# Performance work log

Hardware: AMD Instinct MI355X
Metric: run time of the kernel (lower is better)

Reference implementation:

```python
import jax, jax.numpy as jnp
import numpy as np

H = 64; H2 = 32; B = 256; NPART = 64
NP = B * NPART          # 16384 part nodes
PER_TF = 512            # torque/force nodes per graph
NT = B * PER_TF; NF = NT
E = 262144              # edges per edge type
L = 5; T = 4            # 4 main hetero layers + 1 actor layer; 4 edge types
NEG = 0.2; EPS = 1e-5


def _seg_softmax(e, seg, n):
    # softmax over entries sharing the same segment id (along axis 0)
    m = jax.lax.stop_gradient(jax.ops.segment_max(e, seg, num_segments=n))
    ex = jnp.exp(e - m[seg])
    s = jax.ops.segment_sum(ex, seg, num_segments=n)
    return ex / s[seg]


def _gat(x_s, x_d, es, ed, Ws, Wd, a_s, a_d, b, n_dst):
    # PyG GATConv, heads=1, add_self_loops=False, bipartite (x_src, x_dst)
    hs = x_s @ Ws                      # [Ns,H]
    hd = x_d @ Wd                      # [Nd,H]
    e = jax.nn.leaky_relu((hs @ a_s)[es] + (hd @ a_d)[ed], NEG)   # [E]
    al = _seg_softmax(e, ed, n_dst)                                # attn per dst neighborhood
    return jax.ops.segment_sum(al[:, None] * hs[es], ed, num_segments=n_dst) + b


def _hetero_layer(xp, xt, xf, edges, Ws, Wd, a_s, a_d, b):
    # to_hetero(aggr='sum'): one GATConv per edge type, sum into each dst type
    (pts, ptd), (tps, tpd), (pfs, pfd), (fps, fpd) = edges
    out_t = _gat(xp, xt, pts, ptd, Ws[0], Wd[0], a_s[0], a_d[0], b[0], xt.shape[0])
    out_p = (_gat(xt, xp, tps, tpd, Ws[1], Wd[1], a_s[1], a_d[1], b[1], xp.shape[0])
             + _gat(xf, xp, fps, fpd, Ws[3], Wd[3], a_s[3], a_d[3], b[3], xp.shape[0]))
    out_f = _gat(xp, xf, pfs, pfd, Ws[2], Wd[2], a_s[2], a_d[2], b[2], xf.shape[0])
    return out_p, out_t, out_f


def _pool(x):
    # MultiAggregation([max, min, mean]); segments are uniform -> reshape
    xr = x.reshape(B, -1, x.shape[-1])
    return jnp.concatenate([xr.max(1), xr.min(1), xr.mean(1)], axis=-1)


def reference(mass, part_state, torque_x, force_x,
              e_pt_src, e_pt_dst, e_tp_src, e_tp_dst,
              e_pf_src, e_pf_dst, e_fp_src, e_fp_dst,
              batch, part_id,
              emb_parts_W, emb_state, W_src, W_dst, a_src, a_dst, b_conv,
              ln_gamma, ln_beta, out_a_W, out_a_b,
              innet_W, innet_b, full_W, full_b, outnet_W, outnet_b):
    edges = ((e_pt_src, e_pt_dst), (e_tp_src, e_tp_dst),
             (e_pf_src, e_pf_dst), (e_fp_src, e_fp_dst))
    idx = part_state[:, 0] + 2 * part_state[:, 1]
    xp = jnp.concatenate([mass @ emb_parts_W, emb_state[idx]], axis=-1)  # [NP,H]
    xt, xf = torque_x, force_x
    for l in range(4):  # main hetero GAT, ReLU between layers, none after last
        xp, xt, xf = _hetero_layer(xp, xt, xf, edges,
                                   W_src[l], W_dst[l], a_src[l], a_dst[l], b_conv[l])
        if l < 3:
            xp, xt, xf = jax.nn.relu(xp), jax.nn.relu(xt), jax.nn.relu(xf)
    # actor: 1-layer hetero GAT (no activation)
    ap, at, af = _hetero_layer(xp, xt, xf, edges,
                               W_src[4], W_dst[4], a_src[4], a_dst[4], b_conv[4])
    # node LayerNorm
    mu = ap.mean(-1, keepdims=True)
    var = ((ap - mu) ** 2).mean(-1, keepdims=True)
    ra = (ap - mu) / jnp.sqrt(var + EPS) * ln_gamma + ln_beta
    ra = ra @ out_a_W + out_a_b                         # [NP,2]
    soft = _seg_softmax(ra, batch, B)                   # softmax per graph, per channel
    actions = jnp.zeros((B, 2, NPART), dtype=ra.dtype).at[batch, :, part_id].set(soft)
    actions = actions.reshape(B, 2 * NPART)
    rep = jnp.concatenate([_pool(xp), _pool(xt), _pool(xf)], axis=1)   # [B, 9H]
    repV = jax.nn.gelu(rep @ innet_W + innet_b, approximate=False)
    repV = jax.nn.gelu(repV @ full_W + full_b, approximate=False)
    V = jnp.tanh(repV @ outnet_W + outnet_b)            # [B,1]
    return actions, V


def setup_inputs():
    key = jax.random.key(0)
    ks = iter(jax.random.split(key, 40))
    f32 = jnp.float32
    inp = {}
    inp['mass'] = jax.random.uniform(next(ks), (NP, 1), dtype=f32)
    inp['part_state'] = jax.random.randint(next(ks), (NP, 2), 0, 2, dtype=jnp.int32)
    inp['torque_x'] = jax.random.normal(next(ks), (NT, H), dtype=f32)
    inp['force_x'] = jax.random.normal(next(ks), (NF, H), dtype=f32)
    for name, n in [('e_pt_src', NP), ('e_pt_dst', NT), ('e_tp_src', NT), ('e_tp_dst', NP),
                    ('e_pf_src', NP), ('e_pf_dst', NF), ('e_fp_src', NF), ('e_fp_dst', NP)]:
        inp[name] = jax.random.randint(next(ks), (E,), 0, n, dtype=jnp.int32)
    inp['batch'] = (jnp.arange(NP) // NPART).astype(jnp.int32)
    inp['part_id'] = (jnp.arange(NP) % NPART).astype(jnp.int32)
    s = 1.0 / np.sqrt(H)
    inp['emb_parts_W'] = jax.random.normal(next(ks), (1, H2), dtype=f32)
    inp['emb_state'] = jax.random.normal(next(ks), (4, H2), dtype=f32)
    inp['W_src'] = jax.random.normal(next(ks), (L, T, H, H), dtype=f32) * s
    inp['W_dst'] = jax.random.normal(next(ks), (L, T, H, H), dtype=f32) * s
    inp['a_src'] = jax.random.normal(next(ks), (L, T, H), dtype=f32) * s
    inp['a_dst'] = jax.random.normal(next(ks), (L, T, H), dtype=f32) * s
    inp['b_conv'] = jax.random.normal(next(ks), (L, T, H), dtype=f32) * 0.01
    inp['ln_gamma'] = jnp.ones((H,), dtype=f32)
    inp['ln_beta'] = jnp.zeros((H,), dtype=f32)
    inp['out_a_W'] = jax.random.normal(next(ks), (H, 2), dtype=f32) * s
    inp['out_a_b'] = jnp.zeros((2,), dtype=f32)
    inp['innet_W'] = jax.random.normal(next(ks), (9 * H, H), dtype=f32) / np.sqrt(9.0 * H)
    inp['innet_b'] = jnp.zeros((H,), dtype=f32)
    inp['full_W'] = jax.random.normal(next(ks), (H, H), dtype=f32) * s
    inp['full_b'] = jnp.zeros((H,), dtype=f32)
    inp['outnet_W'] = jax.random.normal(next(ks), (H, 1), dtype=f32) * s
    inp['outnet_b'] = jnp.zeros((1,), dtype=f32)
    return inp
```

## Files before the change

kernel.cpp:

```cpp
#include <hip/hip_runtime.h>
#include <math.h>

#define NP_ 16384
#define NT_ 131072
#define NF_ 131072
#define E_  262144
#define B_  256
#define NDTOT 294912
#define E4_  1048576

#define D0 0
#define D1 131072
#define D2 147456
#define D3 278528
#define S0 0
#define S1 16384
#define S2 147456
#define S3 163840

__device__ __forceinline__ float dot4(float4 a, float4 b) {
  return a.x * b.x + a.y * b.y + a.z * b.z + a.w * b.w;
}

__device__ __forceinline__ void gather2(
    int kb0, int ke0, float ad0, const float* __restrict__ aS0, const float* __restrict__ x0,
    int kb1, int ke1, float ad1, const float* __restrict__ aS1, const float* __restrict__ x1,
    const int* __restrict__ sortsrc, int q, int lanebase,
    float4* __restrict__ acc0o, float* __restrict__ si0o,
    float4* __restrict__ acc1o, float* __restrict__ si1o) {
  float4 acc0 = make_float4(0.f, 0.f, 0.f, 0.f);
  float4 acc1 = make_float4(0.f, 0.f, 0.f, 0.f);
  float m0 = -3e38f, m1 = -3e38f, sum0 = 0.f, sum1 = 0.f;
  int len = max(ke0 - kb0, ke1 - kb1);
  for (int c = 0; c < len; c += 16) {
    int k0 = kb0 + c + q, k1 = kb1 + c + q;
    int v0 = k0 < ke0, v1 = k1 < ke1;
    int sx0 = v0 ? sortsrc[k0] : 0;
    int sx1 = v1 ? sortsrc[k1] : 0;
    float e0 = -3e38f, e1 = -3e38f;
    if (v0) { float t = aS0[sx0] + ad0; e0 = t > 0.f ? t : 0.2f * t; }
    if (v1) { float t = aS1[sx1] + ad1; e1 = t > 0.f ? t : 0.2f * t; }
    float cm0 = e0, cm1 = e1;
#pragma unroll
    for (int off = 1; off < 16; off <<= 1) {
      cm0 = fmaxf(cm0, __shfl_xor(cm0, off));
      cm1 = fmaxf(cm1, __shfl_xor(cm1, off));
    }
    float mn0 = fmaxf(m0, cm0), mn1 = fmaxf(m1, cm1);
    float w0 = v0 ? __expf(e0 - mn0) : 0.f;
    float w1 = v1 ? __expf(e1 - mn1) : 0.f;
    float ws0 = w0, ws1 = w1;
#pragma unroll
    for (int off = 1; off < 16; off <<= 1) {
      ws0 += __shfl_xor(ws0, off);
      ws1 += __shfl_xor(ws1, off);
    }
    float r0 = __expf(m0 - mn0), r1 = __expf(m1 - mn1);
    sum0 = sum0 * r0 + ws0;
    sum1 = sum1 * r1 + ws1;
    acc0.x *= r0; acc0.y *= r0; acc0.z *= r0; acc0.w *= r0;
    acc1.x *= r1; acc1.y *= r1; acc1.z *= r1; acc1.w *= r1;
    int cnt0 = ke0 - (kb0 + c); cnt0 = cnt0 < 0 ? 0 : (cnt0 > 16 ? 16 : cnt0);
    int cnt1 = ke1 - (kb1 + c); cnt1 = cnt1 < 0 ? 0 : (cnt1 > 16 ? 16 : cnt1);
    int cmax = max(cnt0, cnt1);
    for (int i = 0; i < cmax; i += 4) {
      float wa0 = __shfl(w0, lanebase + i, 64);
      float wa1 = __shfl(w0, lanebase + i + 1, 64);
      float wa2 = __shfl(w0, lanebase + i + 2, 64);
      float wa3 = __shfl(w0, lanebase + i + 3, 64);
      int sa0 = __shfl(sx0, lanebase + i, 64);
      int sa1 = __shfl(sx0, lanebase + i + 1, 64);
      int sa2 = __shfl(sx0, lanebase + i + 2, 64);
      int sa3 = __shfl(sx0, lanebase + i + 3, 64);
      float wb0 = __shfl(w1, lanebase + i, 64);
      float wb1 = __shfl(w1, lanebase + i + 1, 64);
      float wb2 = __shfl(w1, lanebase + i + 2, 64);
      float wb3 = __shfl(w1, lanebase + i + 3, 64);
      int sb0 = __shfl(sx1, lanebase + i, 64);
      int sb1 = __shfl(sx1, lanebase + i + 1, 64);
      int sb2 = __shfl(sx1, lanebase + i + 2, 64);
      int sb3 = __shfl(sx1, lanebase + i + 3, 64);
      float4 xa0 = *(const float4*)(x0 + (size_t)sa0 * 64 + q * 4);
      float4 xa1 = *(const float4*)(x0 + (size_t)sa1 * 64 + q * 4);
      float4 xa2 = *(const float4*)(x0 + (size_t)sa2 * 64 + q * 4);
      float4 xa3 = *(const float4*)(x0 + (size_t)sa3 * 64 + q * 4);
      float4 xb0 = *(const float4*)(x1 + (size_t)sb0 * 64 + q * 4);
      float4 xb1 = *(const float4*)(x1 + (size_t)sb1 * 64 + q * 4);
      float4 xb2 = *(const float4*)(x1 + (size_t)sb2 * 64 + q * 4);
      float4 xb3 = *(const float4*)(x1 + (size_t)sb3 * 64 + q * 4);
      acc0.x += wa0 * xa0.x + wa1 * xa1.x + wa2 * xa2.x + wa3 * xa3.x;
      acc0.y += wa0 * xa0.y + wa1 * xa1.y + wa2 * xa2.y + wa3 * xa3.y;
      acc0.z += wa0 * xa0.z + wa1 * xa1.z + wa2 * xa2.z + wa3 * xa3.z;
      acc0.w += wa0 * xa0.w + wa1 * xa1.w + wa2 * xa2.w + wa3 * xa3.w;
      acc1.x += wb0 * xb0.x + wb1 * xb1.x + wb2 * xb2.x + wb3 * xb3.x;
      acc1.y += wb0 * xb0.y + wb1 * xb1.y + wb2 * xb2.y + wb3 * xb3.y;
      acc1.z += wb0 * xb0.z + wb1 * xb1.z + wb2 * xb2.z + wb3 * xb3.z;
      acc1.w += wb0 * xb0.w + wb1 * xb1.w + wb2 * xb2.w + wb3 * xb3.w;
    }
    m0 = mn0; m1 = mn1;
  }
  *si0o = (sum0 > 0.f) ? 1.f / sum0 : 0.f;
  *si1o = (sum1 > 0.f) ? 1.f / sum1 : 0.f;
  *acc0o = acc0;
  *acc1o = acc1;
}

__global__ void k_wa(const float* __restrict__ Wsrc, const float* __restrict__ Wdst,
                     const float* __restrict__ asrc, const float* __restrict__ adst,
                     float* __restrict__ wsas, float* __restrict__ wdad) {
  int b = blockIdx.x;
  int lt = b >> 1;
  int role = b & 1;
  int k = threadIdx.x;
  const float* W = (role == 0 ? Wsrc : Wdst) + ((size_t)(lt * 64 + k)) * 64;
  const float* a = (role == 0 ? asrc : adst) + lt * 64;
  float s = 0.f;
  for (int i = 0; i < 64; i++) s += W[i] * a[i];
  (role == 0 ? wsas : wdad)[lt * 64 + k] = s;
}

__global__ __launch_bounds__(256) void k_build_xp(const float* __restrict__ mass,
    const int* __restrict__ ps, const float* __restrict__ embW,
    const float* __restrict__ embS, const float* __restrict__ wsas,
    const float* __restrict__ wdad, float* __restrict__ xp,
    float* __restrict__ aS, float* __restrict__ aD) {
  int tid = threadIdx.x;
  int n = blockIdx.x * 16 + (tid >> 4);
  int q = tid & 15;
  float4 v;
  if (q < 8) {
    float mv = mass[n];
    const float* e = embW + q * 4;
    v.x = mv * e[0]; v.y = mv * e[1]; v.z = mv * e[2]; v.w = mv * e[3];
  } else {
    int idx = ps[n * 2] + 2 * ps[n * 2 + 1];
    const float4* e = (const float4*)(embS + idx * 32 + (q - 8) * 4);
    v = *e;
  }
  *(float4*)(xp + (size_t)n * 64 + q * 4) = v;
  float4 w0 = *(const float4*)(wsas + 0 * 64 + q * 4);
  float4 w2 = *(const float4*)(wsas + 2 * 64 + q * 4);
  float4 d1 = *(const float4*)(wdad + 1 * 64 + q * 4);
  float4 d3 = *(const float4*)(wdad + 3 * 64 + q * 4);
  float p0 = dot4(v, w0), p2 = dot4(v, w2), p1 = dot4(v, d1), p3 = dot4(v, d3);
#pragma unroll
  for (int off = 1; off < 16; off <<= 1) {
    p0 += __shfl_xor(p0, off); p2 += __shfl_xor(p2, off);
    p1 += __shfl_xor(p1, off); p3 += __shfl_xor(p3, off);
  }
  if (q == 0) { aS[S0 + n] = p0; aS[S2 + n] = p2; aD[D1 + n] = p1; aD[D3 + n] = p3; }
}

__global__ __launch_bounds__(256) void k_init_dots(const float* __restrict__ tx,
    const float* __restrict__ fx, const float* __restrict__ wsas,
    const float* __restrict__ wdad, float* __restrict__ aS, float* __restrict__ aD) {
  int tid = threadIdx.x;
  int q = tid & 15, slot = tid >> 4;
  int b = blockIdx.x;
  int isF = (b >= 8192);
  int n = (isF ? b - 8192 : b) * 16 + slot;
  const float* src = (isF ? fx : tx) + (size_t)n * 64 + q * 4;
  float4 v = *(const float4*)src;
  int tsrc = isF ? 3 : 1, tdst = isF ? 2 : 0;
  float4 ws = *(const float4*)(wsas + tsrc * 64 + q * 4);
  float4 wd = *(const float4*)(wdad + tdst * 64 + q * 4);
  float pS = dot4(v, ws), pD = dot4(v, wd);
#pragma unroll
  for (int off = 1; off < 16; off <<= 1) {
    pS += __shfl_xor(pS, off); pD += __shfl_xor(pD, off);
  }
  if (q == 0) {
    if (!isF) { aS[S1 + n] = pS; aD[D0 + n] = pD; }
    else      { aS[S3 + n] = pS; aD[D2 + n] = pD; }
  }
}

__global__ __launch_bounds__(256) void k_count(
    const int* __restrict__ d0, const int* __restrict__ d1,
    const int* __restrict__ d2, const int* __restrict__ d3,
    int* __restrict__ counts) {
  __shared__ int cnt[64];
  int b = blockIdx.x;
  int t = b >> 6, c = b & 63;
  const int* dp = (t == 0) ? d0 : (t == 1) ? d1 : (t == 2) ? d2 : d3;
  int sh = (t & 1) ? 8 : 11;
  int tid = threadIdx.x;
  if (tid < 64) cnt[tid] = 0;
  __syncthreads();
  const int4* dp4 = (const int4*)dp + (size_t)c * 1024;
  for (int i = tid; i < 1024; i += 256) {
    int4 v = dp4[i];
    atomicAdd(&cnt[v.x >> sh], 1);
    atomicAdd(&cnt[v.y >> sh], 1);
    atomicAdd(&cnt[v.z >> sh], 1);
    atomicAdd(&cnt[v.w >> sh], 1);
  }
  __syncthreads();
  if (tid < 64) counts[(b << 6) + tid] = cnt[tid];
}

__global__ __launch_bounds__(256) void k_bases(const int* __restrict__ counts,
    int* __restrict__ cbase, int* __restrict__ granBase, int* __restrict__ rowptr) {
  __shared__ int tot[256];
  int tid = threadIdx.x;
  int t = tid >> 6, g = tid & 63;
  int s = 0;
  for (int c = 0; c < 64; c++) s += counts[(((t << 6) | c) << 6) + g];
  tot[tid] = s;
  __syncthreads();
  for (int off = 1; off < 256; off <<= 1) {
    int x = 0; if (tid >= off) x = tot[tid - off];
    __syncthreads(); tot[tid] += x; __syncthreads();
  }
  int gb = tot[tid] - s;
  granBase[tid] = gb;
  if (tid == 255) granBase[256] = E4_;
  if (tid == 0) rowptr[NDTOT] = E4_;
  int run = gb;
  for (int c = 0; c < 64; c++) {
    int idx = (((t << 6) | c) << 6) + g;
    int v = counts[idx];
    cbase[idx] = run;
    run += v;
  }
}

__global__ __launch_bounds__(256) void k_place(
    const int* __restrict__ d0, const int* __restrict__ s0,
    const int* __restrict__ d1, const int* __restrict__ s1,
    const int* __restrict__ d2, const int* __restrict__ s2,
    const int* __restrict__ d3, const int* __restrict__ s3,
    const int* __restrict__ cbase, int2* __restrict__ pairs) {
  __shared__ int cur[64];
  int b = blockIdx.x;
  int t = b >> 6, c = b & 63;
  const int* dp; const int* sp;
  if (t == 0) { dp = d0; sp = s0; }
  else if (t == 1) { dp = d1; sp = s1; }
  else if (t == 2) { dp = d2; sp = s2; }
  else { dp = d3; sp = s3; }
  int sh = (t & 1) ? 8 : 11;
  int tid = threadIdx.x;
  if (tid < 64) cur[tid] = cbase[(b << 6) + tid];
  __syncthreads();
  const int4* dp4 = (const int4*)dp + (size_t)c * 1024;
  const int4* sp4 = (const int4*)sp + (size_t)c * 1024;
  for (int i = tid; i < 1024; i += 256) {
    int4 d = dp4[i];
    int4 s = sp4[i];
    int pos;
    pos = atomicAdd(&cur[d.x >> sh], 1); pairs[pos] = make_int2(d.x, s.x);
    pos = atomicAdd(&cur[d.y >> sh], 1); pairs[pos] = make_int2(d.y, s.y);
    pos = atomicAdd(&cur[d.z >> sh], 1); pairs[pos] = make_int2(d.z, s.z);
    pos = atomicAdd(&cur[d.w >> sh], 1); pairs[pos] = make_int2(d.w, s.w);
  }
}

__global__ __launch_bounds__(256) void k_build(const int2* __restrict__ pairs,
    const int* __restrict__ granBase, int* __restrict__ rowptr,
    int* __restrict__ sortsrc) {
  __shared__ int cnt[2048];
  __shared__ int psum[256];
  int g = blockIdx.x;
  int t = g >> 6, gg = g & 63;
  int rows = (t & 1) ? 256 : 2048;
  int rowLo = gg * rows;
  int csr0;
  if (t == 0) csr0 = D0 + rowLo;
  else if (t == 1) csr0 = D1 + rowLo;
  else if (t == 2) csr0 = D2 + rowLo;
  else csr0 = D3 + rowLo;
  int eb = granBase[g], ee = granBase[g + 1];
  int tid = threadIdx.x;
  for (int i = tid; i < rows; i += 256) cnt[i] = 0;
  __syncthreads();
  for (int i = eb + tid; i < ee; i += 256) {
    int2 p = pairs[i];
    atomicAdd(&cnt[p.x - rowLo], 1);
  }
  __syncthreads();
  int per = rows >> 8;
  int b0 = tid * per;
  int s = 0;
  for (int j = 0; j < per; j++) s += cnt[b0 + j];
  psum[tid] = s;
  __syncthreads();
  for (int off = 1; off < 256; off <<= 1) {
    int x = 0; if (tid >= off) x = psum[tid - off];
    __syncthreads(); psum[tid] += x; __syncthreads();
  }
  int run = psum[tid] - s;
  for (int j = 0; j < per; j++) {
    int v = cnt[b0 + j];
    cnt[b0 + j] = run;
    rowptr[csr0 + b0 + j] = eb + run;
    run += v;
  }
  __syncthreads();
  for (int i = eb + tid; i < ee; i += 256) {
    int2 p = pairs[i];
    int pos = eb + atomicAdd(&cnt[p.x - rowLo], 1);
    sortsrc[pos] = p.y;
  }
}

__global__ __launch_bounds__(256) void k_part_hs(int l, const float* __restrict__ Wsrc,
    const float* __restrict__ bconv, const float* __restrict__ xt,
    const float* __restrict__ xf, const float* __restrict__ xp,
    const int* __restrict__ rowptr, const int* __restrict__ sortsrc,
    const float* __restrict__ aSrd, const float* __restrict__ aDrd,
    float* __restrict__ aSwr, float* __restrict__ aDwr,
    const float* __restrict__ wsas, const float* __restrict__ wdad,
    float* __restrict__ xpo, float* __restrict__ hs0, float* __restrict__ hs2,
    int relu, int writeDots,
    const float* __restrict__ gamma, const float* __restrict__ beta,
    const float* __restrict__ oaW, const float* __restrict__ oab,
    float* __restrict__ raOut) {
  __shared__ float Wl[4096];
  __shared__ float shC[2176];
  int tid = threadIdx.x;

  if (blockIdx.x >= NP_ / 16) {
    int b = blockIdx.x - NP_ / 16;
    const float4* W0g = (const float4*)(Wsrc + (size_t)(l * 4 + 0) * 4096);
    const float4* W2g = (const float4*)(Wsrc + (size_t)(l * 4 + 2) * 4096);
#pragma unroll
    for (int i = 0; i < 4; i++) ((float4*)Wl)[i * 256 + tid] = W0g[i * 256 + tid];
    int rlocal = tid >> 4, q = tid & 15;
    int n = b * 16 + rlocal;
    float4 xv = *(const float4*)(xp + (size_t)n * 64 + q * 4);
    *(float4*)(shC + rlocal * 68 + q * 4) = xv;
    __syncthreads();
    const float* xr = shC + rlocal * 68;
    const float4* Wc = (const float4*)Wl;
    float4 o0 = make_float4(0.f, 0.f, 0.f, 0.f);
#pragma unroll 4
    for (int k4 = 0; k4 < 16; k4++) {
      float4 a4 = *(const float4*)(xr + k4 * 4);
#pragma unroll
      for (int kk = 0; kk < 4; kk++) {
        float av = kk == 0 ? a4.x : kk == 1 ? a4.y : kk == 2 ? a4.z : a4.w;
        float4 w0 = Wc[(k4 * 4 + kk) * 16 + q];
        o0.x += av * w0.x; o0.y += av * w0.y; o0.z += av * w0.z; o0.w += av * w0.w;
      }
    }
    *(float4*)(hs0 + (size_t)n * 64 + q * 4) = o0;
    __syncthreads();
#pragma unroll
    for (int i = 0; i < 4; i++) ((float4*)Wl)[i * 256 + tid] = W2g[i * 256 + tid];
    __syncthreads();
    float4 o2 = make_float4(0.f, 0.f, 0.f, 0.f);
#pragma unroll 4
    for (int k4 = 0; k4 < 16; k4++) {
      float4 a4 = *(const float4*)(xr + k4 * 4);
#pragma unroll
      for (int kk = 0; kk < 4; kk++) {
        float av = kk == 0 ? a4.x : kk == 1 ? a4.y : kk == 2 ? a4.z : a4.w;
        float4 w2 = Wc[(k4 * 4 + kk) * 16 + q];
        o2.x += av * w2.x; o2.y += av * w2.y; o2.z += av * w2.z; o2.w += av * w2.w;
      }
    }
    *(float4*)(hs2 + (size_t)n * 64 + q * 4) = o2;
    return;
  }

  float* rowA = shC; float* rowB = shC + 1088;
  const float4* W1g = (const float4*)(Wsrc + (size_t)(l * 4 + 1) * 4096);
  const float4* W3g = (const float4*)(Wsrc + (size_t)(l * 4 + 3) * 4096);
#pragma unroll
  for (int i = 0; i < 4; i++) ((float4*)Wl)[i * 256 + tid] = W1g[i * 256 + tid];

  int rlocal = tid >> 4;
  int q = tid & 15;
  int lanebase = (tid & 63) & 48;
  int n = blockIdx.x * 16 + rlocal;
  int row1 = D1 + n;
  int row3 = D3 + n;

  {
    int kb1 = rowptr[row1], ke1 = rowptr[row1 + 1];
    int kb3 = rowptr[row3], ke3 = rowptr[row3 + 1];
    float4 accA, accB; float siA, siB;
    gather2(kb1, ke1, aDrd[row1], aSrd + S1, xt,
            kb3, ke3, aDrd[row3], aSrd + S3, xf,
            sortsrc, q, lanebase, &accA, &siA, &accB, &siB);
    accA.x *= siA; accA.y *= siA; accA.z *= siA; accA.w *= siA;
    accB.x *= siB; accB.y *= siB; accB.z *= siB; accB.w *= siB;
    *(float4*)(rowA + rlocal * 68 + q * 4) = accA;
    *(float4*)(rowB + rlocal * 68 + q * 4) = accB;
  }
  __syncthreads();

  const float* b1 = bconv + (l * 4 + 1) * 64;
  const float* b3 = bconv + (l * 4 + 3) * 64;
  float4 o = *(const float4*)(b1 + q * 4);
  float4 o3b = *(const float4*)(b3 + q * 4);
  o.x += o3b.x; o.y += o3b.y; o.z += o3b.z; o.w += o3b.w;
  const float4* Wc = (const float4*)Wl;
#pragma unroll 4
  for (int k4 = 0; k4 < 16; k4++) {
    float4 a4 = *(const float4*)(rowA + rlocal * 68 + k4 * 4);
#pragma unroll
    for (int kk = 0; kk < 4; kk++) {
      float av = kk == 0 ? a4.x : kk == 1 ? a4.y : kk == 2 ? a4.z : a4.w;
      float4 w1 = Wc[(k4 * 4 + kk) * 16 + q];
      o.x += av * w1.x; o.y += av * w1.y; o.z += av * w1.z; o.w += av * w1.w;
    }
  }
  __syncthreads();
#pragma unroll
  for (int i = 0; i < 4; i++) ((float4*)Wl)[i * 256 + tid] = W3g[i * 256 + tid];
  __syncthreads();
#pragma unroll 4
  for (int k4 = 0; k4 < 16; k4++) {
    float4 b4 = *(const float4*)(rowB + rlocal * 68 + k4 * 4);
#pragma unroll
    for (int kk = 0; kk < 4; kk++) {
      float bv = kk == 0 ? b4.x : kk == 1 ? b4.y : kk == 2 ? b4.z : b4.w;
      float4 w3 = Wc[(k4 * 4 + kk) * 16 + q];
      o.x += bv * w3.x; o.y += bv * w3.y; o.z += bv * w3.z; o.w += bv * w3.w;
    }
  }

  if (raOut) {
    float ssum = o.x + o.y + o.z + o.w;
#pragma unroll
    for (int off = 1; off < 16; off <<= 1) ssum += __shfl_xor(ssum, off);
    float mean = ssum * (1.f / 64.f);
    float dx = o.x - mean, dy = o.y - mean, dz = o.z - mean, dw = o.w - mean;
    float v2 = dx * dx + dy * dy + dz * dz + dw * dw;
#pragma unroll
    for (int off = 1; off < 16; off <<= 1) v2 += __shfl_xor(v2, off);
    float rstd = 1.f / sqrtf(v2 * (1.f / 64.f) + 1e-5f);
    float4 g4 = *(const float4*)(gamma + q * 4);
    float4 be4 = *(const float4*)(beta + q * 4);
    float y0 = dx * rstd * g4.x + be4.x;
    float y1 = dy * rstd * g4.y + be4.y;
    float y2 = dz * rstd * g4.z + be4.z;
    float y3 = dw * rstd * g4.w + be4.w;
    float4 wA = *(const float4*)(oaW + q * 8);
    float4 wB = *(const float4*)(oaW + q * 8 + 4);
    float p0 = y0 * wA.x + y1 * wA.z + y2 * wB.x + y3 * wB.z;
    float p1 = y0 * wA.y + y1 * wA.w + y2 * wB.y + y3 * wB.w;
#pragma unroll
    for (int off = 1; off < 16; off <<= 1) {
      p0 += __shfl_xor(p0, off);
      p1 += __shfl_xor(p1, off);
    }
    if (q == 0) {
      raOut[(size_t)n * 2]     = p0 + oab[0];
      raOut[(size_t)n * 2 + 1] = p1 + oab[1];
    }
    return;
  }

  if (relu) { o.x = fmaxf(o.x, 0.f); o.y = fmaxf(o.y, 0.f); o.z = fmaxf(o.z, 0.f); o.w = fmaxf(o.w, 0.f); }
  *(float4*)(xpo + (size_t)n * 64 + q * 4) = o;

  if (writeDots) {
    float4 w0 = *(const float4*)(wsas + (size_t)((l + 1) * 4 + 0) * 64 + q * 4);
    float4 w2 = *(const float4*)(wsas + (size_t)((l + 1) * 4 + 2) * 64 + q * 4);
    float4 d1 = *(const float4*)(wdad + (size_t)((l + 1) * 4 + 1) * 64 + q * 4);
    float4 d3 = *(const float4*)(wdad + (size_t)((l + 1) * 4 + 3) * 64 + q * 4);
    float p0 = dot4(o, w0), p2 = dot4(o, w2), p1 = dot4(o, d1), p3 = dot4(o, d3);
#pragma unroll
    for (int off = 1; off < 16; off <<= 1) {
      p0 += __shfl_xor(p0, off); p2 += __shfl_xor(p2, off);
      p1 += __shfl_xor(p1, off); p3 += __shfl_xor(p3, off);
    }
    if (q == 0) { aSwr[S0 + n] = p0; aSwr[S2 + n] = p2; aDwr[D1 + n] = p1; aDwr[D3 + n] = p3; }
  }
}

__global__ __launch_bounds__(256) void k_tf(int l, const float* __restrict__ hs0,
    const float* __restrict__ hs2, const float* __restrict__ bconv,
    const int* __restrict__ rowptr, const int* __restrict__ sortsrc,
    const float* __restrict__ aSrd, const float* __restrict__ aDrd,
    float* __restrict__ aSwr, float* __restrict__ aDwr,
    const float* __restrict__ wsas, const float* __restrict__ wdad,
    float* __restrict__ xt, float* __restrict__ xf, int relu) {
  int tid = threadIdx.x;
  int q = tid & 15, slot = tid >> 4;
  int lanebase = (tid & 63) & 48;
  int b = blockIdx.x;
  int isF = (b >= 4096);
  int rg0 = (isF ? b - 4096 : b) * 32 + slot;
  int rg1 = rg0 + 16;
  int csr0 = (isF ? D2 : D0) + rg0;
  int csr1 = csr0 + 16;
  const float* hs = isF ? hs2 : hs0;
  const float* aSseg = aSrd + (isF ? S2 : S0);
  int t = isF ? 2 : 0;

  int kb0 = rowptr[csr0], ke0 = rowptr[csr0 + 1];
  int kb1 = rowptr[csr1], ke1 = rowptr[csr1 + 1];
  float4 acc0, acc1; float si0, si1;
  gather2(kb0, ke0, aDrd[csr0], aSseg, hs,
          kb1, ke1, aDrd[csr1], aSseg, hs,
          sortsrc, q, lanebase, &acc0, &si0, &acc1, &si1);

  float4 bias = *(const float4*)(bconv + (size_t)(l * 4 + t) * 64 + q * 4);
  float4 o0, o1;
  o0.x = acc0.x * si0 + bias.x; o0.y = acc0.y * si0 + bias.y;
  o0.z = acc0.z * si0 + bias.z; o0.w = acc0.w * si0 + bias.w;
  o1.x = acc1.x * si1 + bias.x; o1.y = acc1.y * si1 + bias.y;
  o1.z = acc1.z * si1 + bias.z; o1.w = acc1.w * si1 + bias.w;
  if (relu) {
    o0.x = fmaxf(o0.x, 0.f); o0.y = fmaxf(o0.y, 0.f);
    o0.z = fmaxf(o0.z, 0.f); o0.w = fmaxf(o0.w, 0.f);
    o1.x = fmaxf(o1.x, 0.f); o1.y = fmaxf(o1.y, 0.f);
    o1.z = fmaxf(o1.z, 0.f); o1.w = fmaxf(o1.w, 0.f);
  }
  float* xout = isF ? xf : xt;
  *(float4*)(xout + (size_t)rg0 * 64 + q * 4) = o0;
  *(float4*)(xout + (size_t)rg1 * 64 + q * 4) = o1;

  int tsrc = isF ? 3 : 1, tdst = isF ? 2 : 0;
  float4 wsv = *(const float4*)(wsas + (size_t)((l + 1) * 4 + tsrc) * 64 + q * 4);
  float4 wdv = *(const float4*)(wdad + (size_t)((l + 1) * 4 + tdst) * 64 + q * 4);
  float pS0 = dot4(o0, wsv), pD0 = dot4(o0, wdv);
  float pS1 = dot4(o1, wsv), pD1 = dot4(o1, wdv);
#pragma unroll
  for (int off = 1; off < 16; off <<= 1) {
    pS0 += __shfl_xor(pS0, off); pD0 += __shfl_xor(pD0, off);
    pS1 += __shfl_xor(pS1, off); pD1 += __shfl_xor(pD1, off);
  }
  if (q == 0) {
    if (!isF) {
      aSwr[S1 + rg0] = pS0; aDwr[D0 + rg0] = pD0;
      aSwr[S1 + rg1] = pS1; aDwr[D0 + rg1] = pD1;
    } else {
      aSwr[S3 + rg0] = pS0; aDwr[D2 + rg0] = pD0;
      aSwr[S3 + rg1] = pS1; aDwr[D2 + rg1] = pD1;
    }
  }
}

__global__ __launch_bounds__(64) void k_actor(const float* __restrict__ ra,
                                              float* __restrict__ outp) {
  int g = blockIdx.x;
  int p = threadIdx.x;
  float2 rv = *(const float2*)(ra + (size_t)(g * 64 + p) * 2);
  float m0 = rv.x, m1 = rv.y;
  for (int off = 32; off > 0; off >>= 1) {
    m0 = fmaxf(m0, __shfl_xor(m0, off));
    m1 = fmaxf(m1, __shfl_xor(m1, off));
  }
  float e0 = __expf(rv.x - m0), e1 = __expf(rv.y - m1);
  float s0 = e0, s1 = e1;
  for (int off = 32; off > 0; off >>= 1) {
    s0 += __shfl_xor(s0, off);
    s1 += __shfl_xor(s1, off);
  }
  outp[g * 128 + p] = e0 / s0;
  outp[g * 128 + 64 + p] = e1 / s1;
}

__global__ __launch_bounds__(256) void k_pool(const float* __restrict__ xp,
    const float* __restrict__ xt, const float* __restrict__ xf,
    float* __restrict__ pool) {
  __shared__ float pmax[4][64], pmin[4][64], psum[4][64];
  int b = blockIdx.x;
  int g = b / 9, c = b % 9;
  int tid = threadIdx.x;
  int grp = tid >> 6, col = tid & 63;
  const float* src; int R;
  if (c == 0)      { src = xp + (size_t)g * 64 * 64; R = 64; }
  else if (c <= 4) { src = xt + ((size_t)g * 512 + (size_t)(c - 1) * 128) * 64; R = 128; }
  else             { src = xf + ((size_t)g * 512 + (size_t)(c - 5) * 128) * 64; R = 128; }
  float mx = -3e38f, mn = 3e38f, sm = 0.f;
  for (int r = grp; r < R; r += 4) {
    float v = src[(size_t)r * 64 + col];
    mx = fmaxf(mx, v); mn = fminf(mn, v); sm += v;
  }
  pmax[grp][col] = mx; pmin[grp][col] = mn; psum[grp][col] = sm;
  __syncthreads();
  if (grp == 0) {
    float M = fmaxf(fmaxf(pmax[0][col], pmax[1][col]), fmaxf(pmax[2][col], pmax[3][col]));
    float m = fminf(fminf(pmin[0][col], pmin[1][col]), fminf(pmin[2][col], pmin[3][col]));
    float S = psum[0][col] + psum[1][col] + psum[2][col] + psum[3][col];
    float* o = pool + ((size_t)(g * 9 + c) * 3) * 64;
    o[col] = M; o[64 + col] = m; o[128 + col] = S;
  }
}

__global__ __launch_bounds__(256) void k_vhead(const float* __restrict__ pool,
    const float* __restrict__ inW, const float* __restrict__ inb,
    const float* __restrict__ fW, const float* __restrict__ fb,
    const float* __restrict__ oW, const float* __restrict__ ob,
    float* __restrict__ outV) {
  __shared__ float rep[576];
  __shared__ float red[256];
  __shared__ float h1[64];
  int g = blockIdx.x, tid = threadIdx.x;
  if (tid < 64) {
    int col = tid;
    const float* pg = pool + (size_t)g * 9 * 3 * 64;
    rep[col] = pg[col];
    rep[64 + col] = pg[64 + col];
    rep[128 + col] = pg[128 + col] * (1.f / 64.f);
    float M = -3e38f, m = 3e38f, S = 0.f;
    for (int c = 1; c <= 4; c++) {
      const float* p = pg + (size_t)c * 192;
      M = fmaxf(M, p[col]); m = fminf(m, p[64 + col]); S += p[128 + col];
    }
    rep[192 + col] = M; rep[256 + col] = m; rep[320 + col] = S * (1.f / 512.f);
    M = -3e38f; m = 3e38f; S = 0.f;
    for (int c = 5; c <= 8; c++) {
      const float* p = pg + (size_t)c * 192;
      M = fmaxf(M, p[col]); m = fminf(m, p[64 + col]); S += p[128 + col];
    }
    rep[384 + col] = M; rep[448 + col] = m; rep[512 + col] = S * (1.f / 512.f);
  }
  __syncthreads();
  const float ISQ2 = 0.70710678118654752f;
  {
    int j = tid & 63, p = tid >> 6;
    float s = 0.f;
    for (int k = p * 144; k < (p + 1) * 144; k++) s += rep[k] * inW[k * 64 + j];
    red[tid] = s;
  }
  __syncthreads();
  if (tid < 64) {
    float s = red[tid] + red[64 + tid] + red[128 + tid] + red[192 + tid] + inb[tid];
    h1[tid] = 0.5f * s * (1.f + erff(s * ISQ2));
  }
  __syncthreads();
  if (tid < 64) {
    float s = fb[tid];
    for (int k = 0; k < 64; k++) s += h1[k] * fW[k * 64 + tid];
    float h2 = 0.5f * s * (1.f + erff(s * ISQ2));
    float p = h2 * oW[tid];
    for (int off = 32; off > 0; off >>= 1) p += __shfl_xor(p, off);
    if (tid == 0) outV[g] = tanhf(p + ob[0]);
  }
}

extern "C" void kernel_launch(void* const* d_in, const int* in_sizes, int n_in,
                              void* d_out, int out_size, void* d_ws, size_t ws_size,
                              hipStream_t stream) {
  (void)in_sizes; (void)n_in; (void)out_size; (void)ws_size;
  const float* mass = (const float*)d_in[0];
  const int*   ps   = (const int*)d_in[1];
  const float* torque_x = (const float*)d_in[2];
  const float* force_x  = (const float*)d_in[3];
  const int* ept_s = (const int*)d_in[4];  const int* ept_d = (const int*)d_in[5];
  const int* etp_s = (const int*)d_in[6];  const int* etp_d = (const int*)d_in[7];
  const int* epf_s = (const int*)d_in[8];  const int* epf_d = (const int*)d_in[9];
  const int* efp_s = (const int*)d_in[10]; const int* efp_d = (const int*)d_in[11];
  const float* embW  = (const float*)d_in[14];
  const float* embS  = (const float*)d_in[15];
  const float* Wsrc  = (const float*)d_in[16];
  const float* Wdst  = (const float*)d_in[17];
  const float* asrc  = (const float*)d_in[18];
  const float* adst  = (const float*)d_in[19];
  const float* bconv = (const float*)d_in[20];
  const float* gamma = (const float*)d_in[21];
  const float* beta  = (const float*)d_in[22];
  const float* oaW   = (const float*)d_in[23];
  const float* oab   = (const float*)d_in[24];
  const float* inW   = (const float*)d_in[25];
  const float* inb   = (const float*)d_in[26];
  const float* fW    = (const float*)d_in[27];
  const float* fb    = (const float*)d_in[28];
  const float* oW    = (const float*)d_in[29];
  const float* ob    = (const float*)d_in[30];

  char* base = (char*)d_ws;
  size_t off = 0;
  auto alloc = [&](size_t bytes) -> void* {
    void* r = base + off;
    off = (off + bytes + 255) & ~(size_t)255;
    return r;
  };
  float* xp0 = (float*)alloc((size_t)NP_ * 64 * 4);
  float* xp1 = (float*)alloc((size_t)NP_ * 64 * 4);
  float* xt  = (float*)alloc((size_t)NT_ * 64 * 4);
  float* xf  = (float*)alloc((size_t)NF_ * 64 * 4);
  float* hs0 = (float*)alloc((size_t)NP_ * 64 * 4);
  float* hs2 = (float*)alloc((size_t)NP_ * 64 * 4);
  float* aSb[2], *aDb[2];
  aSb[0] = (float*)alloc((size_t)NDTOT * 4);
  aSb[1] = (float*)alloc((size_t)NDTOT * 4);
  aDb[0] = (float*)alloc((size_t)NDTOT * 4);
  aDb[1] = (float*)alloc((size_t)NDTOT * 4);
  float* wsas = (float*)alloc(1280 * 4);
  float* wdad = (float*)alloc(1280 * 4);
  float* pool = (float*)alloc((size_t)B_ * 9 * 3 * 64 * 4);
  float* ra   = (float*)alloc((size_t)NP_ * 2 * 4);
  int* rowptr = (int*)alloc((size_t)(NDTOT + 1) * 4);
  int* sortsrc = (int*)alloc((size_t)E4_ * 4);
  int2* pairs  = (int2*)alloc((size_t)E4_ * 8);
  int* counts  = (int*)alloc(16384 * 4);
  int* cbase   = (int*)alloc(16384 * 4);
  int* granBase = (int*)alloc(257 * 4);

  k_wa<<<40, 64, 0, stream>>>(Wsrc, Wdst, asrc, adst, wsas, wdad);
  k_build_xp<<<NP_ / 16, 256, 0, stream>>>(mass, ps, embW, embS, wsas, wdad,
                                           xp0, aSb[0], aDb[0]);
  k_init_dots<<<(NT_ + NF_) / 16, 256, 0, stream>>>(torque_x, force_x,
                                                    wsas, wdad, aSb[0], aDb[0]);
  k_count<<<256, 256, 0, stream>>>(ept_d, etp_d, epf_d, efp_d, counts);
  k_bases<<<1, 256, 0, stream>>>(counts, cbase, granBase, rowptr);
  k_place<<<256, 256, 0, stream>>>(ept_d, ept_s, etp_d, etp_s, epf_d, epf_s,
                                   efp_d, efp_s, cbase, pairs);
  k_build<<<256, 256, 0, stream>>>(pairs, granBase, rowptr, sortsrc);

  float* xpbuf[2] = { xp0, xp1 };
  int cur = 0;
  for (int l = 0; l < 5; l++) {
    int ri = l & 1, wi = (l + 1) & 1;
    int relu = (l < 3) ? 1 : 0;
    const float* xtr = (l == 0) ? torque_x : xt;
    const float* xfr = (l == 0) ? force_x : xf;
    int grid = (l < 4) ? (2 * NP_ / 16) : (NP_ / 16);
    k_part_hs<<<grid, 256, 0, stream>>>(l, Wsrc, bconv, xtr, xfr, xpbuf[cur],
                                        rowptr, sortsrc,
                                        aSb[ri], aDb[ri], aSb[wi], aDb[wi],
                                        wsas, wdad, xpbuf[1 - cur], hs0, hs2,
                                        relu, (l < 4) ? 1 : 0,
                                        gamma, beta, oaW, oab,
                                        (l == 4) ? ra : (float*)nullptr);
    if (l < 4)
      k_tf<<<(NT_ + NF_) / 32, 256, 0, stream>>>(l, hs0, hs2, bconv, rowptr, sortsrc,
                                                 aSb[ri], aDb[ri], aSb[wi], aDb[wi],
                                                 wsas, wdad, xt, xf, relu);
    cur = 1 - cur;
  }

  float* outp = (float*)d_out;
  k_actor<<<B_, 64, 0, stream>>>(ra, outp);
  k_pool<<<B_ * 9, 256, 0, stream>>>(xp0, xt, xf, pool);
  k_vhead<<<B_, 256, 0, stream>>>(pool, inW, inb, fW, fb, oW, ob, outp + B_ * 128);
}
```

Before: 552.5 us.

## Fuse next-layer part projections into part update kernel and split edge types across half-waves

The part-node kernel now gives each 16-lane group one edge type (tp or fp) for a node. The two partial matmul results are combined with a cross-lane shuffle, which doubles parallelism per node and removes the shared-memory staging and block barriers. The separate hs0/hs2 projection blocks are gone: the next layer's source projections are computed in the epilogue of the same kernel, and for layer 0 in k_build_xp, using ping-pong hs buffers. Weights are read straight from global/cache via shuffled activations instead of being staged in LDS. The trade-offs are more global weight traffic per thread and an unguarded read of next-layer dot vectors on the last layer.

```diff
diff --git a/kernel.cpp b/kernel.cpp
--- a/kernel.cpp
+++ b/kernel.cpp
@@ -20,6 +20,63 @@
 
 __device__ __forceinline__ float dot4(float4 a, float4 b) {
   return a.x * b.x + a.y * b.y + a.z * b.z + a.w * b.w;
+}
+
+__device__ __forceinline__ float4 gather_row(int kb, int ke, float ad,
+    const int* __restrict__ sortsrc, const float* __restrict__ aS_seg,
+    const float* __restrict__ xsrc, int q, int lanebase, float* si_out) {
+  float4 acc = make_float4(0.f, 0.f, 0.f, 0.f);
+  float m = -3e38f, ssum = 0.f;
+  for (int base = kb; base < ke; base += 16) {
+    int k = base + q;
+    int valid = (k < ke);
+    int sidx = valid ? sortsrc[k] : 0;
+    float e = -3e38f;
+    if (valid) {
+      e = aS_seg[sidx] + ad;
+      e = e > 0.f ? e : 0.2f * e;
+    }
+    float cm = e;
+#pragma unroll
+    for (int off = 1; off < 16; off <<= 1) cm = fmaxf(cm, __shfl_xor(cm, off));
+    float mn = fmaxf(m, cm);
+    float w = valid ? __expf(e - mn) : 0.f;
+    float ws = w;
+#pragma unroll
+    for (int off = 1; off < 16; off <<= 1) ws += __shfl_xor(ws, off);
+    float r = __expf(m - mn);
+    ssum = ssum * r + ws;
+    acc.x *= r; acc.y *= r; acc.z *= r; acc.w *= r;
+    int cnt = min(16, ke - base);
+    int i = 0;
+    for (; i + 4 <= cnt; i += 4) {
+      float w0 = __shfl(w, lanebase + i, 64);
+      float w1 = __shfl(w, lanebase + i + 1, 64);
+      float w2 = __shfl(w, lanebase + i + 2, 64);
+      float w3 = __shfl(w, lanebase + i + 3, 64);
+      int s0 = __shfl(sidx, lanebase + i, 64);
+      int s1 = __shfl(sidx, lanebase + i + 1, 64);
+      int s2 = __shfl(sidx, lanebase + i + 2, 64);
+      int s3 = __shfl(sidx, lanebase + i + 3, 64);
+      float4 x0 = *(const float4*)(xsrc + (size_t)s0 * 64 + q * 4);
+      float4 x1 = *(const float4*)(xsrc + (size_t)s1 * 64 + q * 4);
+      float4 x2 = *(const float4*)(xsrc + (size_t)s2 * 64 + q * 4);
+      float4 x3 = *(const float4*)(xsrc + (size_t)s3 * 64 + q * 4);
+      acc.x += w0 * x0.x + w1 * x1.x + w2 * x2.x + w3 * x3.x;
+      acc.y += w0 * x0.y + w1 * x1.y + w2 * x2.y + w3 * x3.y;
+      acc.z += w0 * x0.z + w1 * x1.z + w2 * x2.z + w3 * x3.z;
+      acc.w += w0 * x0.w + w1 * x1.w + w2 * x2.w + w3 * x3.w;
+    }
+    for (; i < cnt; i++) {
+      float wi = __shfl(w, lanebase + i, 64);
+      int si = __shfl(sidx, lanebase + i, 64);
+      float4 xv = *(const float4*)(xsrc + (size_t)si * 64 + q * 4);
+      acc.x += wi * xv.x; acc.y += wi * xv.y; acc.z += wi * xv.z; acc.w += wi * xv.w;
+    }
+    m = mn;
+  }
+  *si_out = (ssum > 0.f) ? 1.f / ssum : 0.f;
+  return acc;
 }
 
 __device__ __forceinline__ void gather2(
@@ -121,12 +178,14 @@
 
 __global__ __launch_bounds__(256) void k_build_xp(const float* __restrict__ mass,
     const int* __restrict__ ps, const float* __restrict__ embW,
-    const float* __restrict__ embS, const float* __restrict__ wsas,
-    const float* __restrict__ wdad, float* __restrict__ xp,
+    const float* __restrict__ embS, const float* __restrict__ Wsrc,
+    const float* __restrict__ wsas, const float* __restrict__ wdad,
+    float* __restrict__ hs0, float* __restrict__ hs2,
     float* __restrict__ aS, float* __restrict__ aD) {
   int tid = threadIdx.x;
   int n = blockIdx.x * 16 + (tid >> 4);
   int q = tid & 15;
+  int lanebase = (tid & 63) & 48;
   float4 v;
   if (q < 8) {
     float mv = mass[n];
@@ -137,7 +196,6 @@
     const float4* e = (const float4*)(embS + idx * 32 + (q - 8) * 4);
     v = *e;
   }
-  *(float4*)(xp + (size_t)n * 64 + q * 4) = v;
   float4 w0 = *(const float4*)(wsas + 0 * 64 + q * 4);
   float4 w2 = *(const float4*)(wsas + 2 * 64 + q * 4);
   float4 d1 = *(const float4*)(wdad + 1 * 64 + q * 4);
@@ -149,6 +207,35 @@
     p1 += __shfl_xor(p1, off); p3 += __shfl_xor(p3, off);
   }
   if (q == 0) { aS[S0 + n] = p0; aS[S2 + n] = p2; aD[D1 + n] = p1; aD[D3 + n] = p3; }
+  const float4* W0p = (const float4*)(Wsrc + (size_t)0 * 4096);
+  const float4* W2p = (const float4*)(Wsrc + (size_t)2 * 4096);
+  float4 h0 = make_float4(0.f, 0.f, 0.f, 0.f);
+  float4 h2 = make_float4(0.f, 0.f, 0.f, 0.f);
+#pragma unroll 4
+  for (int k4 = 0; k4 < 16; k4++) {
+    float ax = __shfl(v.x, lanebase + k4, 64);
+    float ay = __shfl(v.y, lanebase + k4, 64);
+    float az = __shfl(v.z, lanebase + k4, 64);
+    float aw = __shfl(v.w, lanebase + k4, 64);
+    float4 a0 = W0p[(k4 * 4 + 0) * 16 + q];
+    float4 a1 = W0p[(k4 * 4 + 1) * 16 + q];
+    float4 a2 = W0p[(k4 * 4 + 2) * 16 + q];
+    float4 a3 = W0p[(k4 * 4 + 3) * 16 + q];
+    float4 c0 = W2p[(k4 * 4 + 0) * 16 + q];
+    float4 c1 = W2p[(k4 * 4 + 1) * 16 + q];
+    float4 c2 = W2p[(k4 * 4 + 2) * 16 + q];
+    float4 c3 = W2p[(k4 * 4 + 3) * 16 + q];
+    h0.x += ax * a0.x + ay * a1.x + az * a2.x + aw * a3.x;
+    h0.y += ax * a0.y + ay * a1.y + az * a2.y + aw * a3.y;
+    h0.z += ax * a0.z + ay * a1.z + az * a2.z + aw * a3.z;
+    h0.w += ax * a0.w + ay * a1.w + az * a2.w + aw * a3.w;
+    h2.x += ax * c0.x + ay * c1.x + az * c2.x + aw * c3.x;
+    h2.y += ax * c0.y + ay * c1.y + az * c2.y + aw * c3.y;
+    h2.z += ax * c0.z + ay * c1.z + az * c2.z + aw * c3.z;
+    h2.w += ax * c0.w + ay * c1.w + az * c2.w + aw * c3.w;
+  }
+  *(float4*)(hs0 + (size_t)n * 64 + q * 4) = h0;
+  *(float4*)(hs2 + (size_t)n * 64 + q * 4) = h2;
 }
 
 __global__ __launch_bounds__(256) void k_init_dots(const float* __restrict__ tx,
@@ -304,123 +391,54 @@
   }
 }
 
-__global__ __launch_bounds__(256) void k_part_hs(int l, const float* __restrict__ Wsrc,
-    const float* __restrict__ bconv, const float* __restrict__ xt,
-    const float* __restrict__ xf, const float* __restrict__ xp,
+__global__ __launch_bounds__(256, 6) void k_part(int l,
+    const float* __restrict__ Wsrc, const float* __restrict__ bconv,
+    const float* __restrict__ xt, const float* __restrict__ xf,
     const int* __restrict__ rowptr, const int* __restrict__ sortsrc,
     const float* __restrict__ aSrd, const float* __restrict__ aDrd,
     float* __restrict__ aSwr, float* __restrict__ aDwr,
     const float* __restrict__ wsas, const float* __restrict__ wdad,
-    float* __restrict__ xpo, float* __restrict__ hs0, float* __restrict__ hs2,
-    int relu, int writeDots,
+    float* __restrict__ xpo, float* __restrict__ hs0n, float* __restrict__ hs2n,
+    int relu, int writeHs,
     const float* __restrict__ gamma, const float* __restrict__ beta,
     const float* __restrict__ oaW, const float* __restrict__ oab,
     float* __restrict__ raOut) {
-  __shared__ float Wl[4096];
-  __shared__ float shC[2176];
-  int tid = threadIdx.x;
-
-  if (blockIdx.x >= NP_ / 16) {
-    int b = blockIdx.x - NP_ / 16;
-    const float4* W0g = (const float4*)(Wsrc + (size_t)(l * 4 + 0) * 4096);
-    const float4* W2g = (const float4*)(Wsrc + (size_t)(l * 4 + 2) * 4096);
-#pragma unroll
-    for (int i = 0; i < 4; i++) ((float4*)Wl)[i * 256 + tid] = W0g[i * 256 + tid];
-    int rlocal = tid >> 4, q = tid & 15;
-    int n = b * 16 + rlocal;
-    float4 xv = *(const float4*)(xp + (size_t)n * 64 + q * 4);
-    *(float4*)(shC + rlocal * 68 + q * 4) = xv;
-    __syncthreads();
-    const float* xr = shC + rlocal * 68;
-    const float4* Wc = (const float4*)Wl;
-    float4 o0 = make_float4(0.f, 0.f, 0.f, 0.f);
-#pragma unroll 4
-    for (int k4 = 0; k4 < 16; k4++) {
-      float4 a4 = *(const float4*)(xr + k4 * 4);
-#pragma unroll
-      for (int kk = 0; kk < 4; kk++) {
-        float av = kk == 0 ? a4.x : kk == 1 ? a4.y : kk == 2 ? a4.z : a4.w;
-        float4 w0 = Wc[(k4 * 4 + kk) * 16 + q];
-        o0.x += av * w0.x; o0.y += av * w0.y; o0.z += av * w0.z; o0.w += av * w0.w;
-      }
-    }
-    *(float4*)(hs0 + (size_t)n * 64 + q * 4) = o0;
-    __syncthreads();
-#pragma unroll
-    for (int i = 0; i < 4; i++) ((float4*)Wl)[i * 256 + tid] = W2g[i * 256 + tid];
-    __syncthreads();
-    float4 o2 = make_float4(0.f, 0.f, 0.f, 0.f);
-#pragma unroll 4
-    for (int k4 = 0; k4 < 16; k4++) {
-      float4 a4 = *(const float4*)(xr + k4 * 4);
-#pragma unroll
-      for (int kk = 0; kk < 4; kk++) {
-        float av = kk == 0 ? a4.x : kk == 1 ? a4.y : kk == 2 ? a4.z : a4.w;
-        float4 w2 = Wc[(k4 * 4 + kk) * 16 + q];
-        o2.x += av * w2.x; o2.y += av * w2.y; o2.z += av * w2.z; o2.w += av * w2.w;
-      }
-    }
-    *(float4*)(hs2 + (size_t)n * 64 + q * 4) = o2;
-    return;
-  }
-
-  float* rowA = shC; float* rowB = shC + 1088;
-  const float4* W1g = (const float4*)(Wsrc + (size_t)(l * 4 + 1) * 4096);
-  const float4* W3g = (const float4*)(Wsrc + (size_t)(l * 4 + 3) * 4096);
-#pragma unroll
-  for (int i = 0; i < 4; i++) ((float4*)Wl)[i * 256 + tid] = W1g[i * 256 + tid];
-
-  int rlocal = tid >> 4;
+  int tid = threadIdx.x;
   int q = tid & 15;
+  int half = (tid >> 4) & 1;
   int lanebase = (tid & 63) & 48;
-  int n = blockIdx.x * 16 + rlocal;
-  int row1 = D1 + n;
-  int row3 = D3 + n;
-
-  {
-    int kb1 = rowptr[row1], ke1 = rowptr[row1 + 1];
-    int kb3 = rowptr[row3], ke3 = rowptr[row3 + 1];
-    float4 accA, accB; float siA, siB;
-    gather2(kb1, ke1, aDrd[row1], aSrd + S1, xt,
-            kb3, ke3, aDrd[row3], aSrd + S3, xf,
-            sortsrc, q, lanebase, &accA, &siA, &accB, &siB);
-    accA.x *= siA; accA.y *= siA; accA.z *= siA; accA.w *= siA;
-    accB.x *= siB; accB.y *= siB; accB.z *= siB; accB.w *= siB;
-    *(float4*)(rowA + rlocal * 68 + q * 4) = accA;
-    *(float4*)(rowB + rlocal * 68 + q * 4) = accB;
-  }
-  __syncthreads();
-
-  const float* b1 = bconv + (l * 4 + 1) * 64;
-  const float* b3 = bconv + (l * 4 + 3) * 64;
-  float4 o = *(const float4*)(b1 + q * 4);
-  float4 o3b = *(const float4*)(b3 + q * 4);
-  o.x += o3b.x; o.y += o3b.y; o.z += o3b.z; o.w += o3b.w;
-  const float4* Wc = (const float4*)Wl;
+  int n = blockIdx.x * 8 + (tid >> 5);
+  int row = (half ? D3 : D1) + n;
+  const float* xsrc = half ? xf : xt;
+  const float* aSseg = aSrd + (half ? S3 : S1);
+
+  int kb = rowptr[row], ke = rowptr[row + 1];
+  float si;
+  float4 acc = gather_row(kb, ke, aDrd[row], sortsrc, aSseg, xsrc, q, lanebase, &si);
+  acc.x *= si; acc.y *= si; acc.z *= si; acc.w *= si;
+
+  const float* bsel = bconv + (size_t)(l * 4 + (half ? 3 : 1)) * 64;
+  float4 o = *(const float4*)(bsel + q * 4);
+  const float4* Wp = (const float4*)(Wsrc + (size_t)(l * 4 + (half ? 3 : 1)) * 4096);
 #pragma unroll 4
   for (int k4 = 0; k4 < 16; k4++) {
-    float4 a4 = *(const float4*)(rowA + rlocal * 68 + k4 * 4);
-#pragma unroll
-    for (int kk = 0; kk < 4; kk++) {
-      float av = kk == 0 ? a4.x : kk == 1 ? a4.y : kk == 2 ? a4.z : a4.w;
-      float4 w1 = Wc[(k4 * 4 + kk) * 16 + q];
-      o.x += av * w1.x; o.y += av * w1.y; o.z += av * w1.z; o.w += av * w1.w;
-    }
-  }
-  __syncthreads();
-#pragma unroll
-  for (int i = 0; i < 4; i++) ((float4*)Wl)[i * 256 + tid] = W3g[i * 256 + tid];
-  __syncthreads();
-#pragma unroll 4
-  for (int k4 = 0; k4 < 16; k4++) {
-    float4 b4 = *(const float4*)(rowB + rlocal * 68 + k4 * 4);
-#pragma unroll
-    for (int kk = 0; kk < 4; kk++) {
-      float bv = kk == 0 ? b4.x : kk == 1 ? b4.y : kk == 2 ? b4.z : b4.w;
-      float4 w3 = Wc[(k4 * 4 + kk) * 16 + q];
-      o.x += bv * w3.x; o.y += bv * w3.y; o.z += bv * w3.z; o.w += bv * w3.w;
-    }
-  }
+    float ax = __shfl(acc.x, lanebase + k4, 64);
+    float ay = __shfl(acc.y, lanebase + k4, 64);
+    float az = __shfl(acc.z, lanebase + k4, 64);
+    float aw = __shfl(acc.w, lanebase + k4, 64);
+    float4 w0 = Wp[(k4 * 4 + 0) * 16 + q];
+    float4 w1 = Wp[(k4 * 4 + 1) * 16 + q];
+    float4 w2 = Wp[(k4 * 4 + 2) * 16 + q];
+    float4 w3 = Wp[(k4 * 4 + 3) * 16 + q];
+    o.x += ax * w0.x + ay * w1.x + az * w2.x + aw * w3.x;
+    o.y += ax * w0.y + ay * w1.y + az * w2.y + aw * w3.y;
+    o.z += ax * w0.z + ay * w1.z + az * w2.z + aw * w3.z;
+    o.w += ax * w0.w + ay * w1.w + az * w2.w + aw * w3.w;
+  }
+  o.x += __shfl_xor(o.x, 16, 64);
+  o.y += __shfl_xor(o.y, 16, 64);
+  o.z += __shfl_xor(o.z, 16, 64);
+  o.w += __shfl_xor(o.w, 16, 64);
 
   if (raOut) {
     float ssum = o.x + o.y + o.z + o.w;
@@ -447,7 +465,7 @@
       p0 += __shfl_xor(p0, off);
       p1 += __shfl_xor(p1, off);
     }
-    if (q == 0) {
+    if (half == 0 && q == 0) {
       raOut[(size_t)n * 2]     = p0 + oab[0];
       raOut[(size_t)n * 2 + 1] = p1 + oab[1];
     }
@@ -455,20 +473,44 @@
   }
 
   if (relu) { o.x = fmaxf(o.x, 0.f); o.y = fmaxf(o.y, 0.f); o.z = fmaxf(o.z, 0.f); o.w = fmaxf(o.w, 0.f); }
-  *(float4*)(xpo + (size_t)n * 64 + q * 4) = o;
-
-  if (writeDots) {
-    float4 w0 = *(const float4*)(wsas + (size_t)((l + 1) * 4 + 0) * 64 + q * 4);
-    float4 w2 = *(const float4*)(wsas + (size_t)((l + 1) * 4 + 2) * 64 + q * 4);
-    float4 d1 = *(const float4*)(wdad + (size_t)((l + 1) * 4 + 1) * 64 + q * 4);
-    float4 d3 = *(const float4*)(wdad + (size_t)((l + 1) * 4 + 3) * 64 + q * 4);
-    float p0 = dot4(o, w0), p2 = dot4(o, w2), p1 = dot4(o, d1), p3 = dot4(o, d3);
+  if (half == 0) *(float4*)(xpo + (size_t)n * 64 + q * 4) = o;
+
+  if (writeHs) {
+    const float4* Wn = (const float4*)(Wsrc + (size_t)((l + 1) * 4 + (half ? 2 : 0)) * 4096);
+    float4 h = make_float4(0.f, 0.f, 0.f, 0.f);
+#pragma unroll 4
+    for (int k4 = 0; k4 < 16; k4++) {
+      float ax = __shfl(o.x, lanebase + k4, 64);
+      float ay = __shfl(o.y, lanebase + k4, 64);
+      float az = __shfl(o.z, lanebase + k4, 64);
+      float aw = __shfl(o.w, lanebase + k4, 64);
+      float4 w0 = Wn[(k4 * 4 + 0) * 16 + q];
+      float4 w1 = Wn[(k4 * 4 + 1) * 16 + q];
+      float4 w2 = Wn[(k4 * 4 + 2) * 16 + q];
+      float4 w3 = Wn[(k4 * 4 + 3) * 16 + q];
+      h.x += ax * w0.x + ay * w1.x + az * w2.x + aw * w3.x;
+      h.y += ax * w0.y + ay * w1.y + az * w2.y + aw * w3.y;
+      h.z += ax * w0.z + ay * w1.z + az * w2.z + aw * w3.z;
+      h.w += ax * w0.w + ay * w1.w + az * w2.w + aw * w3.w;
+    }
+    float* hdst = half ? hs2n : hs0n;
+    *(float4*)(hdst + (size_t)n * 64 + q * 4) = h;
+  }
+
+  {
+    const float* vS = wsas + (size_t)((l + 1) * 4 + (half ? 2 : 0)) * 64;
+    const float* vD = wdad + (size_t)((l + 1) * 4 + (half ? 3 : 1)) * 64;
+    float4 aSv = *(const float4*)(vS + q * 4);
+    float4 aDv = *(const float4*)(vD + q * 4);
+    float pA = dot4(o, aSv), pB = dot4(o, aDv);
 #pragma unroll
     for (int off = 1; off < 16; off <<= 1) {
-      p0 += __shfl_xor(p0, off); p2 += __shfl_xor(p2, off);
-      p1 += __shfl_xor(p1, off); p3 += __shfl_xor(p3, off);
-    }
-    if (q == 0) { aSwr[S0 + n] = p0; aSwr[S2 + n] = p2; aDwr[D1 + n] = p1; aDwr[D3 + n] = p3; }
+      pA += __shfl_xor(pA, off); pB += __shfl_xor(pB, off);
+    }
+    if (q == 0) {
+      if (half == 0) { aSwr[S0 + n] = pA; aDwr[D1 + n] = pB; }
+      else           { aSwr[S2 + n] = pA; aDwr[D3 + n] = pB; }
+    }
   }
 }
 
@@ -673,12 +715,14 @@
     off = (off + bytes + 255) & ~(size_t)255;
     return r;
   };
-  float* xp0 = (float*)alloc((size_t)NP_ * 64 * 4);
-  float* xp1 = (float*)alloc((size_t)NP_ * 64 * 4);
+  float* xp  = (float*)alloc((size_t)NP_ * 64 * 4);
   float* xt  = (float*)alloc((size_t)NT_ * 64 * 4);
   float* xf  = (float*)alloc((size_t)NF_ * 64 * 4);
-  float* hs0 = (float*)alloc((size_t)NP_ * 64 * 4);
-  float* hs2 = (float*)alloc((size_t)NP_ * 64 * 4);
+  float* hs0b[2], *hs2b[2];
+  hs0b[0] = (float*)alloc((size_t)NP_ * 64 * 4);
+  hs0b[1] = (float*)alloc((size_t)NP_ * 64 * 4);
+  hs2b[0] = (float*)alloc((size_t)NP_ * 64 * 4);
+  hs2b[1] = (float*)alloc((size_t)NP_ * 64 * 4);
   float* aSb[2], *aDb[2];
   aSb[0] = (float*)alloc((size_t)NDTOT * 4);
   aSb[1] = (float*)alloc((size_t)NDTOT * 4);
@@ -696,8 +740,8 @@
   int* granBase = (int*)alloc(257 * 4);
 
   k_wa<<<40, 64, 0, stream>>>(Wsrc, Wdst, asrc, adst, wsas, wdad);
-  k_build_xp<<<NP_ / 16, 256, 0, stream>>>(mass, ps, embW, embS, wsas, wdad,
-                                           xp0, aSb[0], aDb[0]);
+  k_build_xp<<<NP_ / 16, 256, 0, stream>>>(mass, ps, embW, embS, Wsrc, wsas, wdad,
+                                           hs0b[0], hs2b[0], aSb[0], aDb[0]);
   k_init_dots<<<(NT_ + NF_) / 16, 256, 0, stream>>>(torque_x, force_x,
                                                     wsas, wdad, aSb[0], aDb[0]);
   k_count<<<256, 256, 0, stream>>>(ept_d, etp_d, epf_d, efp_d, counts);
@@ -706,30 +750,28 @@
                                    efp_d, efp_s, cbase, pairs);
   k_build<<<256, 256, 0, stream>>>(pairs, granBase, rowptr, sortsrc);
 
-  float* xpbuf[2] = { xp0, xp1 };
-  int cur = 0;
   for (int l = 0; l < 5; l++) {
     int ri = l & 1, wi = (l + 1) & 1;
     int relu = (l < 3) ? 1 : 0;
     const float* xtr = (l == 0) ? torque_x : xt;
     const float* xfr = (l == 0) ? force_x : xf;
-    int grid = (l < 4) ? (2 * NP_ / 16) : (NP_ / 16);
-    k_part_hs<<<grid, 256, 0, stream>>>(l, Wsrc, bconv, xtr, xfr, xpbuf[cur],
+    k_part<<<NP_ / 8, 256, 0, stream>>>(l, Wsrc, bconv, xtr, xfr,
                                         rowptr, sortsrc,
                                         aSb[ri], aDb[ri], aSb[wi], aDb[wi],
-                                        wsas, wdad, xpbuf[1 - cur], hs0, hs2,
-                                        relu, (l < 4) ? 1 : 0,
+                                        wsas, wdad, xp,
+                                        hs0b[(l + 1) & 1], hs2b[(l + 1) & 1],
+                                        relu, (l < 3) ? 1 : 0,
                                         gamma, beta, oaW, oab,
                                         (l == 4) ? ra : (float*)nullptr);
     if (l < 4)
-      k_tf<<<(NT_ + NF_) / 32, 256, 0, stream>>>(l, hs0, hs2, bconv, rowptr, sortsrc,
+      k_tf<<<(NT_ + NF_) / 32, 256, 0, stream>>>(l, hs0b[l & 1], hs2b[l & 1], bconv,
+                                                 rowptr, sortsrc,
                                                  aSb[ri], aDb[ri], aSb[wi], aDb[wi],
                                                  wsas, wdad, xt, xf, relu);
-    cur = 1 - cur;
   }
 
   float* outp = (float*)d_out;
   k_actor<<<B_, 64, 0, stream>>>(ra, outp);
-  k_pool<<<B_ * 9, 256, 0, stream>>>(xp0, xt, xf, pool);
+  k_pool<<<B_ * 9, 256, 0, stream>>>(xp, xt, xf, pool);
   k_vhead<<<B_, 256, 0, stream>>>(pool, inW, inb, fW, fb, oW, ob, outp + B_ * 128);
 }
```

New measurement: 638.7 us. +15.6%, slower.
